# Kernel tuning notes

Measured on AMD Instinct MI355X. Metric: run time of the kernel, lower is better.

## Reference

```python
import jax, jax.numpy as jnp
import numpy as np


def setup_inputs() -> dict:
    key = jax.random.key(0)
    k1, k2 = jax.random.split(key)
    N, P1, P2, D = 4, 8192, 8192, 3
    source_cloud = jax.random.normal(k1, (N, P1, D), dtype=jnp.float32)
    target_cloud = jax.random.normal(k2, (N, P2, D), dtype=jnp.float32)
    return {"source_cloud": source_cloud, "target_cloud": target_cloud}


def reference(source_cloud, target_cloud):
    # ChamferDistance.forward with defaults:
    #   bidirectional=False, reverse=False -> single-directional x->y
    #   point_reduction='sum', batch_reduction='mean', norm=2, no normals/weights
    x, y = source_cloud, target_cloud  # (N,P1,D), (N,P2,D)
    x2 = jnp.sum(x * x, axis=-1)                       # (N,P1)
    y2 = jnp.sum(y * y, axis=-1)                       # (N,P2)
    xy = jnp.einsum('npd,nqd->npq', x, y)              # (N,P1,P2)
    d2 = x2[:, :, None] + y2[None if False else slice(None), None, :] - 2.0 * xy  # (N,P1,P2)
    # squared L2 distances are non-negative; clamp tiny negatives from the GEMM trick
    nn_d2 = jnp.maximum(jnp.min(d2, axis=-1), 0.0)     # (N,P1) 1-NN squared dist
    per_cloud = jnp.sum(nn_d2, axis=1)                 # point_reduction='sum'
    loss = jnp.mean(per_cloud)                         # batch_reduction='mean'
    return loss
```

## Files before the change

kernel.cpp:

```cpp
#include <hip/hip_runtime.h>
#include <float.h>

typedef float float2v __attribute__((ext_vector_type(2)));
typedef float float4v __attribute__((ext_vector_type(4)));

#define N_BATCH 4
#define P1 8192
#define P2 8192
#define D 3

#define CHUNK 128
#define NCHUNK (P2 / CHUNK)
#define RSRC 8
#define TPB 256
#define SRC_PER_BLK (TPB * RSRC)
#define NSRCBLK (P1 / SRC_PER_BLK)
#define NMIN (N_BATCH * P1)

#define TPB_R 128

__global__ __launch_bounds__(TPB) void chamfer_main(
        const float* __restrict__ src,
        const float* __restrict__ tgt,
        float* __restrict__ ws,
        float* __restrict__ out) {
    const int bid = blockIdx.x;
    const int c   = bid % NCHUNK;
    const int sb  = (bid / NCHUNK) % NSRCBLK;
    const int n   = bid / (NCHUNK * NSRCBLK);
    const int t   = threadIdx.x;

    if (bid == 0 && t == 0) out[0] = 0.0f;

    __shared__ __align__(16) float sX[CHUNK];
    __shared__ __align__(16) float sY[CHUNK];
    __shared__ __align__(16) float sZ[CHUNK];
    __shared__ __align__(16) float sW[CHUNK];

    if (t < CHUNK) {
        const int j = c * CHUNK + t;
        const float* p = tgt + ((size_t)n * P2 + j) * D;
        const float y0 = p[0], y1 = p[1], y2 = p[2];
        sX[t] = -2.0f * y0;
        sY[t] = -2.0f * y1;
        sZ[t] = -2.0f * y2;
        sW[t] = y0 * y0 + y1 * y1 + y2 * y2;
    }
    __syncthreads();

    float2v bx0[RSRC], bx1[RSRC], bx2[RSRC];
    float m[RSRC];
#pragma unroll
    for (int i = 0; i < RSRC; ++i) {
        const int s = sb * SRC_PER_BLK + i * TPB + t;
        const float* p = src + ((size_t)n * P1 + s) * D;
        bx0[i] = (float2v){p[0], p[0]};
        bx1[i] = (float2v){p[1], p[1]};
        bx2[i] = (float2v){p[2], p[2]};
        m[i] = FLT_MAX;
    }

#pragma unroll 2
    for (int jb = 0; jb < CHUNK; jb += 8) {
        const float4v xA = *(const float4v*)&sX[jb];
        const float4v yA = *(const float4v*)&sY[jb];
        const float4v zA = *(const float4v*)&sZ[jb];
        const float4v wA = *(const float4v*)&sW[jb];
        const float4v xB = *(const float4v*)&sX[jb + 4];
        const float4v yB = *(const float4v*)&sY[jb + 4];
        const float4v zB = *(const float4v*)&sZ[jb + 4];
        const float4v wB = *(const float4v*)&sW[jb + 4];
#pragma unroll
        for (int i = 0; i < RSRC; ++i) {
            float2v d;
            d = __builtin_elementwise_fma(bx0[i], xA.xy, wA.xy);
            d = __builtin_elementwise_fma(bx1[i], yA.xy, d);
            d = __builtin_elementwise_fma(bx2[i], zA.xy, d);
            m[i] = fminf(fminf(m[i], d.x), d.y);
            d = __builtin_elementwise_fma(bx0[i], xA.zw, wA.zw);
            d = __builtin_elementwise_fma(bx1[i], yA.zw, d);
            d = __builtin_elementwise_fma(bx2[i], zA.zw, d);
            m[i] = fminf(fminf(m[i], d.x), d.y);
            d = __builtin_elementwise_fma(bx0[i], xB.xy, wB.xy);
            d = __builtin_elementwise_fma(bx1[i], yB.xy, d);
            d = __builtin_elementwise_fma(bx2[i], zB.xy, d);
            m[i] = fminf(fminf(m[i], d.x), d.y);
            d = __builtin_elementwise_fma(bx0[i], xB.zw, wB.zw);
            d = __builtin_elementwise_fma(bx1[i], yB.zw, d);
            d = __builtin_elementwise_fma(bx2[i], zB.zw, d);
            m[i] = fminf(fminf(m[i], d.x), d.y);
        }
    }

#pragma unroll
    for (int i = 0; i < RSRC; ++i) {
        const int s = n * P1 + sb * SRC_PER_BLK + i * TPB + t;
        ws[(size_t)c * NMIN + s] = m[i];
    }
}

__global__ __launch_bounds__(TPB_R) void chamfer_reduce(
        const float* __restrict__ ws,
        const float* __restrict__ src,
        float* __restrict__ out) {
    const int gid = blockIdx.x * TPB_R + threadIdx.x;

    float v[NCHUNK];
#pragma unroll
    for (int c = 0; c < NCHUNK; ++c)
        v[c] = ws[(size_t)c * NMIN + gid];
#pragma unroll
    for (int s = NCHUNK / 2; s > 0; s >>= 1)
#pragma unroll
        for (int c = 0; c < s; ++c)
            v[c] = fminf(v[c], v[c + s]);

    const float* p = src + (size_t)gid * D;
    const float xs = p[0] * p[0] + p[1] * p[1] + p[2] * p[2];
    float r = fmaxf(v[0] + xs, 0.0f);

#pragma unroll
    for (int off = 32; off > 0; off >>= 1)
        r += __shfl_down(r, off, 64);
    __shared__ float sred[TPB_R / 64];
    const int lane = threadIdx.x & 63;
    const int w    = threadIdx.x >> 6;
    if (lane == 0) sred[w] = r;
    __syncthreads();
    if (threadIdx.x == 0) {
        float s = 0.0f;
#pragma unroll
        for (int i = 0; i < TPB_R / 64; ++i) s += sred[i];
        atomicAdd(out, s * (1.0f / N_BATCH));
    }
}

extern "C" void kernel_launch(void* const* d_in, const int* in_sizes, int n_in,
                              void* d_out, int out_size, void* d_ws, size_t ws_size,
                              hipStream_t stream) {
    const float* src = (const float*)d_in[0];
    const float* tgt = (const float*)d_in[1];
    float* out = (float*)d_out;
    float* ws  = (float*)d_ws;

    const int nblocks = N_BATCH * NSRCBLK * NCHUNK;
    chamfer_main<<<nblocks, TPB, 0, stream>>>(src, tgt, ws, out);

    chamfer_reduce<<<NMIN / TPB_R, TPB_R, 0, stream>>>(ws, src, out);
}
```

Baseline: 34.60 us.

## Fuse min-reduce into main kernel via atomicMin and last-block final sum

Replaces the per-chunk workspace write and separate reduction kernel with atomicMin on the float bit patterns of clamped per-point distances, followed by a last-block ticket that sums all minima. RSRC is doubled to 16 with launch bounds of 2, which halves the number of blocks and increases per-thread reuse of target data. Shared-memory target loads are software double-buffered. In exchange it adds a memset launch, heavy atomic traffic (64 atomicMins per source point), and higher register pressure from 16 accumulators.

After: 57.71 us. 1.67x slower.

```diff
diff --git a/kernel.cpp b/kernel.cpp
--- a/kernel.cpp
+++ b/kernel.cpp
@@ -11,18 +11,24 @@
 
 #define CHUNK 128
 #define NCHUNK (P2 / CHUNK)
-#define RSRC 8
+#define NGRP (CHUNK / 8)
+#define RSRC 16
 #define TPB 256
 #define SRC_PER_BLK (TPB * RSRC)
 #define NSRCBLK (P1 / SRC_PER_BLK)
 #define NMIN (N_BATCH * P1)
+#define NBLOCKS (N_BATCH * NSRCBLK * NCHUNK)
 
-#define TPB_R 128
+#define FILLPAT 0x7F7F7F7Fu
+#define LAST_TICKET (FILLPAT + (unsigned)NBLOCKS - 1u)
 
-__global__ __launch_bounds__(TPB) void chamfer_main(
+struct Grp { float4v x[2], y[2], z[2], w[2]; };
+
+__global__ __launch_bounds__(TPB, 2) void chamfer_fused(
         const float* __restrict__ src,
         const float* __restrict__ tgt,
-        float* __restrict__ ws,
+        unsigned* __restrict__ mins,
+        unsigned* __restrict__ cnt,
         float* __restrict__ out) {
     const int bid = blockIdx.x;
     const int c   = bid % NCHUNK;
@@ -30,12 +36,12 @@
     const int n   = bid / (NCHUNK * NSRCBLK);
     const int t   = threadIdx.x;
 
-    if (bid == 0 && t == 0) out[0] = 0.0f;
-
     __shared__ __align__(16) float sX[CHUNK];
     __shared__ __align__(16) float sY[CHUNK];
     __shared__ __align__(16) float sZ[CHUNK];
     __shared__ __align__(16) float sW[CHUNK];
+    __shared__ unsigned sLast;
+    __shared__ float sred[TPB / 64];
 
     if (t < CHUNK) {
         const int j = c * CHUNK + t;
@@ -60,78 +66,74 @@
         m[i] = FLT_MAX;
     }
 
-#pragma unroll 2
-    for (int jb = 0; jb < CHUNK; jb += 8) {
-        const float4v xA = *(const float4v*)&sX[jb];
-        const float4v yA = *(const float4v*)&sY[jb];
-        const float4v zA = *(const float4v*)&sZ[jb];
-        const float4v wA = *(const float4v*)&sW[jb];
-        const float4v xB = *(const float4v*)&sX[jb + 4];
-        const float4v yB = *(const float4v*)&sY[jb + 4];
-        const float4v zB = *(const float4v*)&sZ[jb + 4];
-        const float4v wB = *(const float4v*)&sW[jb + 4];
+    Grp cur;
+    {
+        cur.x[0] = *(const float4v*)&sX[0]; cur.x[1] = *(const float4v*)&sX[4];
+        cur.y[0] = *(const float4v*)&sY[0]; cur.y[1] = *(const float4v*)&sY[4];
+        cur.z[0] = *(const float4v*)&sZ[0]; cur.z[1] = *(const float4v*)&sZ[4];
+        cur.w[0] = *(const float4v*)&sW[0]; cur.w[1] = *(const float4v*)&sW[4];
+    }
+#pragma unroll
+    for (int g = 0; g < NGRP; ++g) {
+        Grp nxt;
+        if (g + 1 < NGRP) {
+            const int jb = (g + 1) * 8;
+            nxt.x[0] = *(const float4v*)&sX[jb]; nxt.x[1] = *(const float4v*)&sX[jb + 4];
+            nxt.y[0] = *(const float4v*)&sY[jb]; nxt.y[1] = *(const float4v*)&sY[jb + 4];
+            nxt.z[0] = *(const float4v*)&sZ[jb]; nxt.z[1] = *(const float4v*)&sZ[jb + 4];
+            nxt.w[0] = *(const float4v*)&sW[jb]; nxt.w[1] = *(const float4v*)&sW[jb + 4];
+        }
 #pragma unroll
         for (int i = 0; i < RSRC; ++i) {
-            float2v d;
-            d = __builtin_elementwise_fma(bx0[i], xA.xy, wA.xy);
-            d = __builtin_elementwise_fma(bx1[i], yA.xy, d);
-            d = __builtin_elementwise_fma(bx2[i], zA.xy, d);
-            m[i] = fminf(fminf(m[i], d.x), d.y);
-            d = __builtin_elementwise_fma(bx0[i], xA.zw, wA.zw);
-            d = __builtin_elementwise_fma(bx1[i], yA.zw, d);
-            d = __builtin_elementwise_fma(bx2[i], zA.zw, d);
-            m[i] = fminf(fminf(m[i], d.x), d.y);
-            d = __builtin_elementwise_fma(bx0[i], xB.xy, wB.xy);
-            d = __builtin_elementwise_fma(bx1[i], yB.xy, d);
-            d = __builtin_elementwise_fma(bx2[i], zB.xy, d);
-            m[i] = fminf(fminf(m[i], d.x), d.y);
-            d = __builtin_elementwise_fma(bx0[i], xB.zw, wB.zw);
-            d = __builtin_elementwise_fma(bx1[i], yB.zw, d);
-            d = __builtin_elementwise_fma(bx2[i], zB.zw, d);
-            m[i] = fminf(fminf(m[i], d.x), d.y);
+#pragma unroll
+            for (int h = 0; h < 2; ++h) {
+                float2v d;
+                d = __builtin_elementwise_fma(bx0[i], cur.x[h].xy, cur.w[h].xy);
+                d = __builtin_elementwise_fma(bx1[i], cur.y[h].xy, d);
+                d = __builtin_elementwise_fma(bx2[i], cur.z[h].xy, d);
+                m[i] = fminf(fminf(m[i], d.x), d.y);
+                d = __builtin_elementwise_fma(bx0[i], cur.x[h].zw, cur.w[h].zw);
+                d = __builtin_elementwise_fma(bx1[i], cur.y[h].zw, d);
+                d = __builtin_elementwise_fma(bx2[i], cur.z[h].zw, d);
+                m[i] = fminf(fminf(m[i], d.x), d.y);
+            }
         }
+        if (g + 1 < NGRP) cur = nxt;
     }
 
 #pragma unroll
     for (int i = 0; i < RSRC; ++i) {
+        const float xs = bx0[i].x * bx0[i].x + bx1[i].x * bx1[i].x
+                       + bx2[i].x * bx2[i].x;
+        const float v = fmaxf(xs + m[i], 0.0f);
         const int s = n * P1 + sb * SRC_PER_BLK + i * TPB + t;
-        ws[(size_t)c * NMIN + s] = m[i];
+        atomicMin(&mins[s], __float_as_uint(v));
     }
-}
 
-__global__ __launch_bounds__(TPB_R) void chamfer_reduce(
-        const float* __restrict__ ws,
-        const float* __restrict__ src,
-        float* __restrict__ out) {
-    const int gid = blockIdx.x * TPB_R + threadIdx.x;
-
-    float v[NCHUNK];
+    __threadfence();
+    if (t == 0) sLast = (atomicAdd(cnt, 1u) == LAST_TICKET) ? 1u : 0u;
+    __syncthreads();
+    if (sLast) {
+        __threadfence();
+        const float4v* mv = (const float4v*)mins;
+        float ssum = 0.0f;
 #pragma unroll
-    for (int c = 0; c < NCHUNK; ++c)
-        v[c] = ws[(size_t)c * NMIN + gid];
+        for (int k = 0; k < NMIN / 4 / TPB; ++k) {
+            const float4v v = mv[(size_t)k * TPB + t];
+            ssum += v.x + v.y + v.z + v.w;
+        }
 #pragma unroll
-    for (int s = NCHUNK / 2; s > 0; s >>= 1)
+        for (int off = 32; off > 0; off >>= 1)
+            ssum += __shfl_down(ssum, off, 64);
+        const int lane = t & 63, w = t >> 6;
+        if (lane == 0) sred[w] = ssum;
+        __syncthreads();
+        if (t == 0) {
+            float s = 0.0f;
 #pragma unroll
-        for (int c = 0; c < s; ++c)
-            v[c] = fminf(v[c], v[c + s]);
-
-    const float* p = src + (size_t)gid * D;
-    const float xs = p[0] * p[0] + p[1] * p[1] + p[2] * p[2];
-    float r = fmaxf(v[0] + xs, 0.0f);
-
-#pragma unroll
-    for (int off = 32; off > 0; off >>= 1)
-        r += __shfl_down(r, off, 64);
-    __shared__ float sred[TPB_R / 64];
-    const int lane = threadIdx.x & 63;
-    const int w    = threadIdx.x >> 6;
-    if (lane == 0) sred[w] = r;
-    __syncthreads();
-    if (threadIdx.x == 0) {
-        float s = 0.0f;
-#pragma unroll
-        for (int i = 0; i < TPB_R / 64; ++i) s += sred[i];
-        atomicAdd(out, s * (1.0f / N_BATCH));
+            for (int i = 0; i < TPB / 64; ++i) s += sred[i];
+            out[0] = s * (1.0f / N_BATCH);
+        }
     }
 }
 
@@ -141,10 +143,10 @@
     const float* src = (const float*)d_in[0];
     const float* tgt = (const float*)d_in[1];
     float* out = (float*)d_out;
-    float* ws  = (float*)d_ws;
+    unsigned* mins = (unsigned*)d_ws;
+    unsigned* cnt  = mins + NMIN;
 
-    const int nblocks = N_BATCH * NSRCBLK * NCHUNK;
-    chamfer_main<<<nblocks, TPB, 0, stream>>>(src, tgt, ws, out);
+    hipMemsetAsync(d_ws, 0x7F, (size_t)NMIN * 4 + 4, stream);
 
-    chamfer_reduce<<<NMIN / TPB_R, TPB_R, 0, stream>>>(ws, src, out);
+    chamfer_fused<<<NBLOCKS, TPB, 0, stream>>>(src, tgt, mins, cnt, out);
 }
```
